# Kernel optimization log

Hardware: AMD Instinct MI355X
Metric: run time of the kernel (lower is better)

Reference implementation:

```python
import jax, jax.numpy as jnp
import numpy as np

N_SPLIT = 4096   # split tokens (coarse octree levels)
N_VQ    = 12288  # VQ tokens (finest level)
N       = N_SPLIT + N_VQ
C       = 256    # num_embed
H       = 8      # num_heads
L       = 4      # num_blocks
P       = 256    # patch_size (attention window)
DIL     = 2      # dilation for odd (swin) blocks
DVQ     = 32     # vqvae embedding_channels
VQ_SIZE = 256    # vqvae embedding_sizes
VQ_G    = 4      # vqvae quantizer_group
HID     = 4 * C


def _layernorm(x, s, b):
    m = x.mean(-1, keepdims=True)
    v = jnp.var(x, axis=-1, keepdims=True)
    return (x - m) * jax.lax.rsqrt(v + 1e-5) * s + b


def _sin_pos_emb(n, c):
    pos = jnp.arange(n, dtype=jnp.float32)[:, None]
    half = c // 2
    freqs = jnp.exp(-jnp.log(10000.0) * jnp.arange(half, dtype=jnp.float32) / half)
    ang = pos * freqs
    return jnp.concatenate([jnp.sin(ang), jnp.cos(ang)], axis=-1)


def _forward(split, zq, targets_vq, category, batch_id, mask, d2b,
             split_emb, class_emb, vq_proj_w, vq_proj_b,
             ln1_s, ln1_b, qkv_w, qkv_b, attn_w, attn_b,
             ln2_s, ln2_b, fc1_w, fc1_b, fc2_w, fc2_b,
             lnx_s, lnx_b, split_w, split_b, vq_w, vq_b):
    # token embeddings: [split tokens ; projected VQ codes]
    x = jnp.concatenate([split_emb[split], zq @ vq_proj_w + vq_proj_b], axis=0)  # [N,C]
    cond = class_emb[category]                      # [B,C]
    x = jnp.where(mask[:, None], cond[batch_id], x)  # masked tokens -> class cond

    # depth2batch gather, then OctFormer blocks
    xb = x[d2b] + _sin_pos_emb(N, C).astype(x.dtype)
    dh = C // H
    scale = dh ** -0.5
    for l in range(L):
        d = DIL if (l % 2 == 1) else 1  # swin-style alternating dilation
        h = _layernorm(xb, ln1_s[l], ln1_b[l])
        # dilated window partition: window j in a super-window holds tokens base+p*d+j
        hw = h.reshape(-1, P, d, C).transpose(0, 2, 1, 3).reshape(-1, P, C)
        qkv = hw @ qkv_w[l] + qkv_b[l]              # [nw,P,3C]
        q, k, v = [t.reshape(-1, P, H, dh) for t in jnp.split(qkv, 3, axis=-1)]
        att = jax.nn.softmax(jnp.einsum('wphd,wqhd->whpq', q, k) * scale, axis=-1)
        o = jnp.einsum('whpq,wqhd->wphd', att, v).reshape(-1, P, C) @ attn_w[l] + attn_b[l]
        o = o.reshape(-1, d, P, C).transpose(0, 2, 1, 3).reshape(-1, C)  # undo partition
        xb = xb + o
        h = _layernorm(xb, ln2_s[l], ln2_b[l])
        xb = xb + (jax.nn.gelu(h @ fc1_w[l] + fc1_b[l]) @ fc2_w[l] + fc2_b[l])
    # batch2depth scatter (inverse permutation)
    x = jnp.zeros_like(xb).at[d2b].set(xb)
    x = _layernorm(x, lnx_s, lnx_b)

    # split head + masked cross-entropy
    sl = x[:N_SPLIT] @ split_w + split_b            # [Ns,2]
    ms = mask[:N_SPLIT].astype(jnp.float32)
    ce_s = -jnp.take_along_axis(jax.nn.log_softmax(sl, axis=-1), split[:, None], axis=-1)[:, 0]
    split_loss = jnp.sum(ce_s * ms) / jnp.maximum(jnp.sum(ms), 1.0)

    # vq head + masked grouped cross-entropy
    vl = (x[N_SPLIT:] @ vq_w + vq_b).reshape(N_VQ, VQ_G, VQ_SIZE)
    mv = mask[N_SPLIT:].astype(jnp.float32)
    ce_v = -jnp.take_along_axis(jax.nn.log_softmax(vl, axis=-1), targets_vq[..., None], axis=-1)[..., 0]
    vq_loss = jnp.sum(ce_v.mean(-1) * mv) / jnp.maximum(jnp.sum(mv), 1.0)
    return jnp.stack([split_loss, vq_loss])


def setup_inputs() -> dict:
    key = jax.random.key(0)
    ks = jax.random.split(key, 16)
    s = 0.02
    inp = {
        'split': jax.random.randint(ks[0], (N_SPLIT,), 0, 2),
        'zq': jax.random.normal(ks[1], (N_VQ, DVQ), jnp.float32),
        'targets_vq': jax.random.randint(ks[2], (N_VQ, VQ_G), 0, VQ_SIZE),
        'category': jnp.zeros((1,), jnp.int32),
        'batch_id': jnp.zeros((N,), jnp.int32),
        'mask': jax.random.randint(ks[3], (N,), 0, 2).astype(bool),
        'd2b': jax.random.permutation(ks[4], N),
        'split_emb': s * jax.random.normal(ks[5], (2, C), jnp.float32),
        'class_emb': s * jax.random.normal(ks[6], (1, C), jnp.float32),
        'vq_proj_w': s * jax.random.normal(ks[7], (DVQ, C), jnp.float32),
        'vq_proj_b': jnp.zeros((C,), jnp.float32),
        'ln1_s': jnp.ones((L, C), jnp.float32),
        'ln1_b': jnp.zeros((L, C), jnp.float32),
        'qkv_w': s * jax.random.normal(ks[8], (L, C, 3 * C), jnp.float32),
        'qkv_b': jnp.zeros((L, 3 * C), jnp.float32),
        'attn_w': s * jax.random.normal(ks[9], (L, C, C), jnp.float32),
        'attn_b': jnp.zeros((L, C), jnp.float32),
        'ln2_s': jnp.ones((L, C), jnp.float32),
        'ln2_b': jnp.zeros((L, C), jnp.float32),
        'fc1_w': s * jax.random.normal(ks[10], (L, C, HID), jnp.float32),
        'fc1_b': jnp.zeros((L, HID), jnp.float32),
        'fc2_w': s * jax.random.normal(ks[11], (L, HID, C), jnp.float32),
        'fc2_b': jnp.zeros((L, C), jnp.float32),
        'lnx_s': jnp.ones((C,), jnp.float32),
        'lnx_b': jnp.zeros((C,), jnp.float32),
        'split_w': s * jax.random.normal(ks[12], (C, 2), jnp.float32),
        'split_b': jnp.zeros((2,), jnp.float32),
        'vq_w': s * jax.random.normal(ks[13], (C, VQ_G * VQ_SIZE), jnp.float32),
        'vq_b': jnp.zeros((VQ_G * VQ_SIZE,), jnp.float32),
    }
    return inp


def reference(split, zq, targets_vq, category, batch_id, mask, d2b,
              split_emb, class_emb, vq_proj_w, vq_proj_b,
              ln1_s, ln1_b, qkv_w, qkv_b, attn_w, attn_b,
              ln2_s, ln2_b, fc1_w, fc1_b, fc2_w, fc2_b,
              lnx_s, lnx_b, split_w, split_b, vq_w, vq_b):
    return _forward(split, zq, targets_vq, category, batch_id, mask, d2b,
                    split_emb, class_emb, vq_proj_w, vq_proj_b,
                    ln1_s, ln1_b, qkv_w, qkv_b, attn_w, attn_b,
                    ln2_s, ln2_b, fc1_w, fc1_b, fc2_w, fc2_b,
                    lnx_s, lnx_b, split_w, split_b, vq_w, vq_b)
```

## Files before the change

### kernel.cpp

```cpp
#include <hip/hip_runtime.h>
#include <hip/hip_bf16.h>
#include <math.h>

#define NSPLIT 4096
#define NVQ    12288
#define NTOK   16384
#define CH     256
#define NH     8
#define DHD    32
#define NL     4
#define PW     256
#define HIDN   1024
#define DVQ    32
#define VQG    4
#define VQS    256

typedef __attribute__((ext_vector_type(8))) short bf16x8;
typedef __attribute__((ext_vector_type(4))) float f32x4;

typedef const __attribute__((address_space(1))) void* gas_ptr;
typedef __attribute__((address_space(3))) void* las_ptr;
#define GLD16(g, s) __builtin_amdgcn_global_load_lds((gas_ptr)(g), (las_ptr)(s), 16, 0, 0)

static __device__ __forceinline__ unsigned pack2bf(float a, float b) {
    __hip_bfloat16 ha = __float2bfloat16(a), hb = __float2bfloat16(b);
    return ((unsigned)*(unsigned short*)&hb << 16) | *(unsigned short*)&ha;
}
static __device__ __forceinline__ float bf2f(unsigned short s) {
    unsigned u = (unsigned)s << 16;
    return *(float*)&u;
}
static __device__ __forceinline__ unsigned short f2bfu(float f) {
    __hip_bfloat16 h = __float2bfloat16(f);
    return *(unsigned short*)&h;
}

__global__ void k_mask(const void* __restrict__ raw, int* __restrict__ mi) {
    __shared__ int c_even, c_odd, c_0100, sh_mode;
    const unsigned short* u16 = (const unsigned short*)raw;
    if (threadIdx.x == 0) { c_even = 0; c_odd = 0; c_0100 = 0; }
    __syncthreads();
    int le = 0, lo = 0, l01 = 0;
    for (int i = threadIdx.x; i < 8192; i += 256) {
        unsigned short v = u16[i];
        if (v == 0x3F80u) { if (i & 1) lo++; else le++; }
        if (v == 0x0100u) l01++;
    }
    atomicAdd(&c_even, le); atomicAdd(&c_odd, lo); atomicAdd(&c_0100, l01);
    __syncthreads();
    if (threadIdx.x == 0) {
        int m;
        if      (c_even > 500) m = 2;
        else if (c_odd  > 500) m = 3;
        else if (c_0100 > 500) m = 1;
        else                   m = 0;
        sh_mode = m;
    }
    __syncthreads();
    int m = sh_mode;
    for (int i = threadIdx.x; i < NTOK; i += 256) {
        int v;
        if      (m == 0) v = ((const int*)raw)[i] != 0;
        else if (m == 1) v = ((const unsigned char*)raw)[i] != 0;
        else if (m == 2) v = ((const unsigned short*)raw)[i] != 0;
        else             v = ((const unsigned int*)raw)[i] != 0;
        mi[i] = v;
    }
}

__global__ void k_wt_all(const float* __restrict__ qkv_w, const float* __restrict__ attn_w,
                         const float* __restrict__ fc1_w, const float* __restrict__ fc2_w,
                         const float* __restrict__ vq_w,
                         short* __restrict__ qkvT, short* __restrict__ attnT,
                         short* __restrict__ fc1T, short* __restrict__ fc2T,
                         short* __restrict__ vqT) {
    int b = blockIdx.x;
    const float* W; short* Wt; int K, N, tn, tk;
    if (b < 192)      { int r = b;       int z = r / 48; r %= 48; K = 256;  N = 768;
                        tk = r / 12; tn = r % 12;
                        W = qkv_w + (size_t)z * K * N; Wt = qkvT + (size_t)z * K * N; }
    else if (b < 256) { int r = b - 192; int z = r / 16; r %= 16; K = 256;  N = 256;
                        tk = r / 4;  tn = r % 4;
                        W = attn_w + (size_t)z * K * N; Wt = attnT + (size_t)z * K * N; }
    else if (b < 512) { int r = b - 256; int z = r / 64; r %= 64; K = 256;  N = 1024;
                        tk = r / 16; tn = r % 16;
                        W = fc1_w + (size_t)z * K * N; Wt = fc1T + (size_t)z * K * N; }
    else if (b < 768) { int r = b - 512; int z = r / 64; r %= 64; K = 1024; N = 256;
                        tk = r / 4;  tn = r % 4;
                        W = fc2_w + (size_t)z * K * N; Wt = fc2T + (size_t)z * K * N; }
    else              { int r = b - 768; K = 256; N = 1024;
                        tk = r / 16; tn = r % 16; W = vq_w; Wt = vqT; }
    __shared__ float t[64][65];
    int bn = tn * 64, bk = tk * 64, tid = threadIdx.x;
#pragma unroll
    for (int it = 0; it < 16; ++it) {
        int idx = it * 256 + tid; int r = idx >> 6, c = idx & 63;
        t[r][c] = W[(size_t)(bk + r) * N + bn + c];
    }
    __syncthreads();
#pragma unroll
    for (int it = 0; it < 16; ++it) {
        int idx = it * 256 + tid; int r = idx >> 6, c = idx & 63;
        __hip_bfloat16 h = __float2bfloat16(t[c][r]);
        Wt[(size_t)(bn + r) * K + bk + c] = *(short*)&h;
    }
}

__global__ void k_embed_gather(const int* __restrict__ split, const float* __restrict__ zq,
                               const int* __restrict__ category, const int* __restrict__ batch_id,
                               const int* __restrict__ mask_i, const int* __restrict__ d2b,
                               const float* __restrict__ split_emb, const float* __restrict__ class_emb,
                               const float* __restrict__ vq_proj_w, const float* __restrict__ vq_proj_b,
                               const float* __restrict__ ln1s, const float* __restrict__ ln1b,
                               unsigned short* __restrict__ xbv, unsigned short* __restrict__ hb) {
    int j = blockIdx.x, c = threadIdx.x;
    int i = d2b[j];
    float v;
    if (mask_i[i]) {
        v = class_emb[category[batch_id[i]] * CH + c];
    } else if (i < NSPLIT) {
        v = split_emb[split[i] * CH + c];
    } else {
        const float* z = zq + (size_t)(i - NSPLIT) * DVQ;
        float acc = vq_proj_b[c];
#pragma unroll
        for (int k = 0; k < DVQ; k++) acc += z[k] * vq_proj_w[k * CH + c];
        v = acc;
    }
    const float kneg = -0.07195578415606394f;
    float jf = (float)j, pe;
    if (c < 128) { float f = expf(c * kneg);         pe = sinf(jf * f); }
    else         { float f = expf((c - 128) * kneg); pe = cosf(jf * f); }
    v += pe;
    float s = v, sq = v * v;
#pragma unroll
    for (int o = 32; o; o >>= 1) { s += __shfl_xor(s, o); sq += __shfl_xor(sq, o); }
    __shared__ float ps[4], pq[4];
    if ((c & 63) == 0) { ps[c >> 6] = s; pq[c >> 6] = sq; }
    __syncthreads();
    float S = ps[0] + ps[1] + ps[2] + ps[3];
    float Q = pq[0] + pq[1] + pq[2] + pq[3];
    float mean = S * (1.0f / CH);
    float var  = Q * (1.0f / CH) - mean * mean;
    float rsf = rsqrtf(var + 1e-5f);
    xbv[(size_t)j * CH + c] = f2bfu(v);
    hb[(size_t)j * CH + c]  = f2bfu((v - mean) * rsf * ln1s[c] + ln1b[c]);
}

template <int GELU>
__global__ __launch_bounds__(256, 4) void k_mm(
    const short* __restrict__ A, const short* __restrict__ Bt,
    const float* __restrict__ bias, __hip_bfloat16* __restrict__ outB,
    int N, int K) {
    __shared__ short As[2][128 * 32];
    __shared__ short Bs[2][128 * 32];
    const int tid = threadIdx.x;
    const int w = tid >> 6, l = tid & 63;
    const int bm = blockIdx.y * 128, bn = blockIdx.x * 128;
    const int wr = w >> 1, wc = w & 1;
    const int q = l >> 4, rA = l & 15;
    const int srow = w * 16 + (l >> 2);
    const int sx = ((l & 3) ^ ((l >> 2) & 3)) * 8;
    const int fx = (q ^ (rA & 3)) * 8;

    const short* gA0 = A + (size_t)(bm + srow) * K + sx;
    const short* gA1 = A + (size_t)(bm + srow + 64) * K + sx;
    const short* gB0 = Bt + (size_t)(bn + srow) * K + sx;
    const short* gB1 = Bt + (size_t)(bn + srow + 64) * K + sx;
    short* lA0 = &As[0][w * 16 * 32];
    short* lA1 = &As[0][(64 + w * 16) * 32];
    short* lA0h = &As[1][w * 16 * 32];
    short* lA1h = &As[1][(64 + w * 16) * 32];
    short* lB0 = &Bs[0][w * 16 * 32];
    short* lB1 = &Bs[0][(64 + w * 16) * 32];
    short* lB0h = &Bs[1][w * 16 * 32];
    short* lB1h = &Bs[1][(64 + w * 16) * 32];

    f32x4 acc[4][4] = {};

    for (int k0 = 0; k0 < K; k0 += 64) {
        GLD16(gA0 + k0, lA0);       GLD16(gA1 + k0, lA1);
        GLD16(gA0 + k0 + 32, lA0h); GLD16(gA1 + k0 + 32, lA1h);
        GLD16(gB0 + k0, lB0);       GLD16(gB1 + k0, lB1);
        GLD16(gB0 + k0 + 32, lB0h); GLD16(gB1 + k0 + 32, lB1h);
        __syncthreads();
#pragma unroll
        for (int s = 0; s < 2; s++) {
            bf16x8 a[4], b[4];
#pragma unroll
            for (int m = 0; m < 4; m++)
                a[m] = *(const bf16x8*)(&As[s][(wr * 64 + m * 16 + rA) * 32 + fx]);
#pragma unroll
            for (int n = 0; n < 4; n++)
                b[n] = *(const bf16x8*)(&Bs[s][(wc * 64 + n * 16 + rA) * 32 + fx]);
#pragma unroll
            for (int m = 0; m < 4; m++)
#pragma unroll
                for (int n = 0; n < 4; n++)
                    acc[m][n] = __builtin_amdgcn_mfma_f32_16x16x32_bf16(a[m], b[n], acc[m][n], 0, 0, 0);
        }
        __syncthreads();
    }

#pragma unroll
    for (int m = 0; m < 4; m++) {
        int row0 = bm + wr * 64 + m * 16 + q * 4;
#pragma unroll
        for (int n = 0; n < 4; n++) {
            int col = bn + wc * 64 + n * 16 + rA;
            float bv = bias[col];
#pragma unroll
            for (int r2 = 0; r2 < 4; r2++) {
                float v = acc[m][n][r2] + bv;
                if (GELU) {
                    float t = tanhf(0.7978845608028654f * (v + 0.044715f * v * v * v));
                    v = 0.5f * v * (1.0f + t);
                }
                outB[(size_t)(row0 + r2) * N + col] = __float2bfloat16(v);
            }
        }
    }
}

template <int LNOUT>
__global__ __launch_bounds__(256, 3) void k_mm_row(
    const short* __restrict__ A, const short* __restrict__ Bt,
    const float* __restrict__ bias, unsigned short* __restrict__ xbv,
    const float* __restrict__ lns, const float* __restrict__ lnb,
    unsigned short* __restrict__ h_out, int K) {
    __shared__ short As[2][64 * 32];
    __shared__ short Bs[2][256 * 32];
    __shared__ float part[2][4][64];
    const int tid = threadIdx.x;
    const int w = tid >> 6, l = tid & 63;
    const int bm = blockIdx.x * 64;
    const int q = l >> 4, rA = l & 15;
    const int sx = ((l & 3) ^ ((l >> 2) & 3)) * 8;
    const int fx = (q ^ (rA & 3)) * 8;

    const short* gA = A + (size_t)(bm + w * 16 + (l >> 2)) * K + sx;
    const short* gB = Bt + (size_t)(w * 64 + (l >> 2)) * K + sx;
    short* lA0 = &As[0][(w * 16) * 32];
    short* lA1 = &As[1][(w * 16) * 32];

    f32x4 acc[4][4] = {};

    for (int k0 = 0; k0 < K; k0 += 64) {
        GLD16(gA + k0, lA0);
        GLD16(gA + k0 + 32, lA1);
#pragma unroll
        for (int i = 0; i < 4; i++) {
            GLD16(gB + (size_t)(i * 16) * K + k0,      &Bs[0][(w * 64 + i * 16) * 32]);
            GLD16(gB + (size_t)(i * 16) * K + k0 + 32, &Bs[1][(w * 64 + i * 16) * 32]);
        }
        __syncthreads();
#pragma unroll
        for (int s = 0; s < 2; s++) {
            bf16x8 a[4], b[4];
#pragma unroll
            for (int m = 0; m < 4; m++)
                a[m] = *(const bf16x8*)(&As[s][(m * 16 + rA) * 32 + fx]);
#pragma unroll
            for (int n = 0; n < 4; n++)
                b[n] = *(const bf16x8*)(&Bs[s][(w * 64 + n * 16 + rA) * 32 + fx]);
#pragma unroll
            for (int m = 0; m < 4; m++)
#pragma unroll
                for (int n = 0; n < 4; n++)
                    acc[m][n] = __builtin_amdgcn_mfma_f32_16x16x32_bf16(a[m], b[n], acc[m][n], 0, 0, 0);
        }
        __syncthreads();
    }

    float rsum[4][4] = {}, rsq[4][4] = {};
#pragma unroll
    for (int m = 0; m < 4; m++) {
#pragma unroll
        for (int n = 0; n < 4; n++) {
            int col = w * 64 + n * 16 + rA;
            float bv = bias[col];
#pragma unroll
            for (int r2 = 0; r2 < 4; r2++) {
                int row = bm + m * 16 + q * 4 + r2;
                size_t oi = (size_t)row * CH + col;
                float v = acc[m][n][r2] + bv + bf2f(xbv[oi]);
                acc[m][n][r2] = v;
                xbv[oi] = f2bfu(v);
                rsum[m][r2] += v;
                rsq[m][r2] += v * v;
            }
        }
    }
    if (LNOUT) {
#pragma unroll
        for (int m = 0; m < 4; m++)
#pragma unroll
            for (int r2 = 0; r2 < 4; r2++) {
#pragma unroll
                for (int o = 8; o; o >>= 1) {
                    rsum[m][r2] += __shfl_xor(rsum[m][r2], o);
                    rsq[m][r2]  += __shfl_xor(rsq[m][r2], o);
                }
            }
        if (rA == 0) {
#pragma unroll
            for (int m = 0; m < 4; m++)
#pragma unroll
                for (int r2 = 0; r2 < 4; r2++) {
                    int row = m * 16 + q * 4 + r2;
                    part[0][w][row] = rsum[m][r2];
                    part[1][w][row] = rsq[m][r2];
                }
        }
        __syncthreads();
#pragma unroll
        for (int m = 0; m < 4; m++) {
#pragma unroll
            for (int r2 = 0; r2 < 4; r2++) {
                int row = m * 16 + q * 4 + r2;
                float S = part[0][0][row] + part[0][1][row] + part[0][2][row] + part[0][3][row];
                float Q = part[1][0][row] + part[1][1][row] + part[1][2][row] + part[1][3][row];
                float mean = S * (1.0f / CH);
                float var  = Q * (1.0f / CH) - mean * mean;
                float rsf = rsqrtf(var + 1e-5f);
#pragma unroll
                for (int n = 0; n < 4; n++) {
                    int col = w * 64 + n * 16 + rA;
                    float h = (acc[m][n][r2] - mean) * rsf * lns[col] + lnb[col];
                    h_out[(size_t)(bm + row) * CH + col] = f2bfu(h);
                }
            }
        }
    }
}

__global__ __launch_bounds__(256) void k_attn_mfma(const short* __restrict__ qkv,
                                                   short* __restrict__ o, int dil) {
    __shared__ short Vt[DHD * PW];
    __shared__ short Pl[4][64 * 64];
    const int wid = blockIdx.x, h = blockIdx.y;
    const int tid = threadIdx.x;
    const int w = tid >> 6, l = tid & 63;
    const int g = l >> 4, c = l & 15;
    const int tbase = (wid / dil) * (PW * dil) + (wid % dil);

    {
        const int p = tid;
        const short* src = qkv + (size_t)(tbase + p * dil) * 768 + 2 * CH + h * DHD;
        bf16x8 v0 = *(const bf16x8*)(src);
        bf16x8 v1 = *(const bf16x8*)(src + 8);
        bf16x8 v2 = *(const bf16x8*)(src + 16);
        bf16x8 v3 = *(const bf16x8*)(src + 24);
        const int pc = p >> 3, po = p & 7;
#pragma unroll
        for (int d = 0; d < 8; d++)  Vt[(d)      * PW + ((pc ^ d) << 3) + po] = v0[d];
#pragma unroll
        for (int d = 0; d < 8; d++)  Vt[(d + 8)  * PW + ((pc ^ d) << 3) + po] = v1[d];
#pragma unroll
        for (int d = 0; d < 8; d++)  Vt[(d + 16) * PW + ((pc ^ d) << 3) + po] = v2[d];
#pragma unroll
        for (int d = 0; d < 8; d++)  Vt[(d + 24) * PW + ((pc ^ d) << 3) + po] = v3[d];
    }

    bf16x8 qf[4];
#pragma unroll
    for (int qt = 0; qt < 4; qt++) {
        int qrow = w * 64 + qt * 16 + c;
        qf[qt] = *(const bf16x8*)(qkv + (size_t)(tbase + qrow * dil) * 768 + h * DHD + g * 8);
    }

    f32x4 acco[4][2] = {};
    float m_s[4] = {-1e30f, -1e30f, -1e30f, -1e30f};
    float l_s[4] = {0.f, 0.f, 0.f, 0.f};
    const float scale = 0.17677669529663687f;

    __syncthreads();

#pragma unroll
    for (int ch = 0; ch < 4; ch++) {
        bf16x8 kf[4];
#pragma unroll
        for (int kvt = 0; kvt < 4; kvt++) {
            int kv = ch * 64 + kvt * 16 + c;
            kf[kvt] = *(const bf16x8*)(qkv + (size_t)(tbase + kv * dil) * 768 + CH + h * DHD + g * 8);
        }
        f32x4 accs[4][4] = {};
#pragma unroll
        for (int kvt = 0; kvt < 4; kvt++)
#pragma unroll
            for (int qt = 0; qt < 4; qt++)
                accs[kvt][qt] = __builtin_amdgcn_mfma_f32_16x16x32_bf16(kf[kvt], qf[qt], accs[kvt][qt], 0, 0, 0);

        float fb[4];
#pragma unroll
        for (int qt = 0; qt < 4; qt++) {
            float mx = -1e30f;
#pragma unroll
            for (int kvt = 0; kvt < 4; kvt++) {
                mx = fmaxf(mx, fmaxf(fmaxf(accs[kvt][qt][0], accs[kvt][qt][1]),
                                     fmaxf(accs[kvt][qt][2], accs[kvt][qt][3])));
            }
            mx = fmaxf(mx, __shfl_xor(mx, 16));
            mx = fmaxf(mx, __shfl_xor(mx, 32));
            float mnew = fmaxf(m_s[qt], mx * scale);
            fb[qt] = __expf(m_s[qt] - mnew);
            m_s[qt] = mnew;
        }
#pragma unroll
        for (int mt = 0; mt < 4; mt++)
#pragma unroll
            for (int r = 0; r < 4; r++) {
                float fo = __shfl(fb[mt], g * 4 + r);
                acco[mt][0][r] *= fo;
                acco[mt][1][r] *= fo;
            }
        float rsum[4] = {0.f, 0.f, 0.f, 0.f};
#pragma unroll
        for (int kvt = 0; kvt < 4; kvt++) {
            const int cchunk = kvt * 2 + (g >> 1);
            const int koff = (g & 1) << 2;
#pragma unroll
            for (int qt = 0; qt < 4; qt++) {
                float p0 = __expf(accs[kvt][qt][0] * scale - m_s[qt]);
                float p1 = __expf(accs[kvt][qt][1] * scale - m_s[qt]);
                float p2 = __expf(accs[kvt][qt][2] * scale - m_s[qt]);
                float p3 = __expf(accs[kvt][qt][3] * scale - m_s[qt]);
                rsum[qt] += (p0 + p1) + (p2 + p3);
                int qq = qt * 16 + c;
                int phys = cchunk ^ (qq & 7);
                uint2 pk; pk.x = pack2bf(p0, p1); pk.y = pack2bf(p2, p3);
                *(uint2*)(&Pl[w][qq * 64 + phys * 8 + koff]) = pk;
            }
        }
#pragma unroll
        for (int qt = 0; qt < 4; qt++) {
            float s = rsum[qt];
            s += __shfl_xor(s, 16);
            s += __shfl_xor(s, 32);
            l_s[qt] = l_s[qt] * fb[qt] + s;
        }
#pragma unroll
        for (int ks = 0; ks < 2; ks++) {
            bf16x8 pa[4];
#pragma unroll
            for (int mt = 0; mt < 4; mt++) {
                int qq = mt * 16 + c;
                int phys = (ks * 4 + g) ^ (qq & 7);
                pa[mt] = *(const bf16x8*)(&Pl[w][qq * 64 + phys * 8]);
            }
#pragma unroll
            for (int nt = 0; nt < 2; nt++) {
                int d = nt * 16 + c;
                int kvabs = ch * 64 + ks * 32 + g * 8;
                int phys = (kvabs >> 3) ^ (d & 7);
                bf16x8 vb = *(const bf16x8*)(&Vt[d * PW + phys * 8]);
#pragma unroll
                for (int mt = 0; mt < 4; mt++)
                    acco[mt][nt] = __builtin_amdgcn_mfma_f32_16x16x32_bf16(pa[mt], vb, acco[mt][nt], 0, 0, 0);
            }
        }
    }

#pragma unroll
    for (int mt = 0; mt < 4; mt++) {
        float linv_own = 1.0f / l_s[mt];
#pragma unroll
        for (int r = 0; r < 4; r++) {
            float linv = __shfl(linv_own, g * 4 + r);
            int qrow = w * 64 + mt * 16 + g * 4 + r;
            size_t trow = (size_t)(tbase + qrow * dil) * CH + h * DHD;
#pragma unroll
            for (int nt = 0; nt < 2; nt++) {
                __hip_bfloat16 hv = __float2bfloat16(acco[mt][nt][r] * linv);
                o[trow + nt * 16 + c] = *(short*)&hv;
            }
        }
    }
}

__global__ void k_lnx_scatter_split(const unsigned short* __restrict__ xbv, const int* __restrict__ d2b,
                                    const float* __restrict__ s, const float* __restrict__ b,
                                    const int* __restrict__ split, const int* __restrict__ mask_i,
                                    const float* __restrict__ sw, const float* __restrict__ sb,
                                    __hip_bfloat16* __restrict__ out,
                                    float* __restrict__ sce, float* __restrict__ smv) {
    int j = blockIdx.x * 4 + (threadIdx.x >> 6);
    int l = threadIdx.x & 63;
    ushort4 uv = *(const ushort4*)(xbv + (size_t)j * CH + l * 4);
    float vx = bf2f(uv.x), vy = bf2f(uv.y), vz = bf2f(uv.z), vw = bf2f(uv.w);
    float sum = vx + vy + vz + vw;
    float sq  = vx * vx + vy * vy + vz * vz + vw * vw;
#pragma unroll
    for (int o = 32; o; o >>= 1) { sum += __shfl_xor(sum, o); sq += __shfl_xor(sq, o); }
    float mean = sum * (1.0f / CH);
    float var  = sq * (1.0f / CH) - mean * mean;
    float rs = rsqrtf(var + 1e-5f);
    float4 sv = *(const float4*)(s + l * 4);
    float4 bv = *(const float4*)(b + l * 4);
    float n0 = (vx - mean) * rs * sv.x + bv.x;
    float n1 = (vy - mean) * rs * sv.y + bv.y;
    float n2 = (vz - mean) * rs * sv.z + bv.z;
    float n3 = (vw - mean) * rs * sv.w + bv.w;
    int i = d2b[j];
    uint2 pk; pk.x = pack2bf(n0, n1); pk.y = pack2bf(n2, n3);
    *(uint2*)((unsigned short*)out + (size_t)i * CH + l * 4) = pk;
    if (i < NSPLIT) {
        int c0 = l * 4;
        float a0 = n0 * sw[2 * c0] + n1 * sw[2 * (c0 + 1)] + n2 * sw[2 * (c0 + 2)] + n3 * sw[2 * (c0 + 3)];
        float a1 = n0 * sw[2 * c0 + 1] + n1 * sw[2 * (c0 + 1) + 1] + n2 * sw[2 * (c0 + 2) + 1] + n3 * sw[2 * (c0 + 3) + 1];
#pragma unroll
        for (int o = 32; o; o >>= 1) { a0 += __shfl_xor(a0, o); a1 += __shfl_xor(a1, o); }
        if (l == 0) {
            float l0 = a0 + sb[0], l1 = a1 + sb[1];
            float mx = fmaxf(l0, l1);
            float lse = mx + logf(__expf(l0 - mx) + __expf(l1 - mx));
            float ce = lse - (split[i] ? l1 : l0);
            float ms = (float)mask_i[i];
            sce[i] = ce * ms;
            smv[i] = ms;
        }
    }
}

__global__ void k_vq_loss(const unsigned short* __restrict__ vl, const int* __restrict__ targets,
                          const int* __restrict__ mask_i, float* __restrict__ vce,
                          float* __restrict__ vmv) {
    int i = blockIdx.x;
    int wv = threadIdx.x >> 6;
    int l = threadIdx.x & 63;
    const unsigned short* row = vl + (size_t)i * (VQG * VQS) + wv * VQS;
    ushort4 v4 = *(const ushort4*)(row + l * 4);
    float e0 = bf2f(v4.x), e1 = bf2f(v4.y), e2 = bf2f(v4.z), e3 = bf2f(v4.w);
    float mx = fmaxf(fmaxf(e0, e1), fmaxf(e2, e3));
#pragma unroll
    for (int o = 32; o; o >>= 1) mx = fmaxf(mx, __shfl_xor(mx, o));
    float s = __expf(e0 - mx) + __expf(e1 - mx) + __expf(e2 - mx) + __expf(e3 - mx);
#pragma unroll
    for (int o = 32; o; o >>= 1) s += __shfl_xor(s, o);
    __shared__ float ce[VQG];
    if (l == 0) ce[wv] = (mx + logf(s)) - bf2f(row[targets[i * VQG + wv]]);
    __syncthreads();
    if (threadIdx.x == 0) {
        float mv = (float)mask_i[NSPLIT + i];
        vce[i] = (ce[0] + ce[1] + ce[2] + ce[3]) * 0.25f * mv;
        vmv[i] = mv;
    }
}

__global__ void k_reduce(const float* __restrict__ sce, const float* __restrict__ smv,
                         const float* __restrict__ vce, const float* __restrict__ vmv,
                         float* __restrict__ out) {
    int tid = threadIdx.x;
    float s1 = 0, s2 = 0, s3 = 0, s4 = 0;
    for (int i = tid; i < NSPLIT; i += 256) { s1 += sce[i]; s2 += smv[i]; }
    for (int i = tid; i < NVQ; i += 256)    { s3 += vce[i]; s4 += vmv[i]; }
    __shared__ float r1[256], r2[256], r3[256], r4[256];
    r1[tid] = s1; r2[tid] = s2; r3[tid] = s3; r4[tid] = s4;
    __syncthreads();
    for (int o = 128; o; o >>= 1) {
        if (tid < o) { r1[tid] += r1[tid + o]; r2[tid] += r2[tid + o];
                       r3[tid] += r3[tid + o]; r4[tid] += r4[tid + o]; }
        __syncthreads();
    }
    if (tid == 0) {
        out[0] = r1[0] / fmaxf(r2[0], 1.0f);
        out[1] = r3[0] / fmaxf(r4[0], 1.0f);
    }
}

extern "C" void kernel_launch(void* const* d_in, const int* in_sizes, int n_in,
                              void* d_out, int out_size, void* d_ws, size_t ws_size,
                              hipStream_t stream) {
    const int*   split      = (const int*)d_in[0];
    const float* zq         = (const float*)d_in[1];
    const int*   targets_vq = (const int*)d_in[2];
    const int*   category   = (const int*)d_in[3];
    const int*   batch_id   = (const int*)d_in[4];
    const void*  mask_raw   = d_in[5];
    const int*   d2b        = (const int*)d_in[6];
    const float* split_emb  = (const float*)d_in[7];
    const float* class_emb  = (const float*)d_in[8];
    const float* vq_proj_w  = (const float*)d_in[9];
    const float* vq_proj_b  = (const float*)d_in[10];
    const float* ln1_s      = (const float*)d_in[11];
    const float* ln1_b      = (const float*)d_in[12];
    const float* qkv_w      = (const float*)d_in[13];
    const float* qkv_b      = (const float*)d_in[14];
    const float* attn_w     = (const float*)d_in[15];
    const float* attn_b     = (const float*)d_in[16];
    const float* ln2_s      = (const float*)d_in[17];
    const float* ln2_b      = (const float*)d_in[18];
    const float* fc1_w      = (const float*)d_in[19];
    const float* fc1_b      = (const float*)d_in[20];
    const float* fc2_w      = (const float*)d_in[21];
    const float* fc2_b      = (const float*)d_in[22];
    const float* lnx_s      = (const float*)d_in[23];
    const float* lnx_b      = (const float*)d_in[24];
    const float* sw         = (const float*)d_in[25];
    const float* sb         = (const float*)d_in[26];
    const float* vq_w       = (const float*)d_in[27];
    const float* vq_b       = (const float*)d_in[28];

    char* ws = (char*)d_ws;
    int* mask_i = (int*)(ws + 256);
    float* sce = (float*)(ws + 256 + 4 * NTOK);
    float* smv = sce + NSPLIT;
    float* vce = smv + NSPLIT;
    float* vmv = vce + NVQ;
    char* p = ws + (1 << 20);
    short* qkvT = (short*)p;  p += (size_t)NL * 768 * CH * 2;
    short* attnT = (short*)p; p += (size_t)NL * CH * CH * 2;
    short* fc1T = (short*)p;  p += (size_t)NL * HIDN * CH * 2;
    short* fc2T = (short*)p;  p += (size_t)NL * CH * HIDN * 2;
    short* vqT = (short*)p;   p += (size_t)HIDN * CH * 2;
    unsigned short* xbv = (unsigned short*)p; p += (size_t)NTOK * CH * 2;
    unsigned short* h_bf = (unsigned short*)p; p += (size_t)NTOK * CH * 2;
    unsigned short* o_bf = (unsigned short*)p; p += (size_t)NTOK * CH * 2;
    short* big = (short*)p;

    k_mask<<<1, 256, 0, stream>>>(mask_raw, mask_i);
    k_wt_all<<<832, 256, 0, stream>>>(qkv_w, attn_w, fc1_w, fc2_w, vq_w,
                                      qkvT, attnT, fc1T, fc2T, vqT);
    k_embed_gather<<<NTOK, 256, 0, stream>>>(split, zq, category, batch_id, mask_i, d2b,
                                             split_emb, class_emb, vq_proj_w, vq_proj_b,
                                             ln1_s, ln1_b, xbv, h_bf);

    for (int l = 0; l < NL; l++) {
        int d = (l & 1) ? 2 : 1;
        k_mm<0><<<dim3(768 / 128, NTOK / 128), 256, 0, stream>>>(
            (const short*)h_bf, qkvT + (size_t)l * 768 * CH, qkv_b + l * 768,
            (__hip_bfloat16*)big, 768, CH);
        k_attn_mfma<<<dim3(NTOK / PW, NH), 256, 0, stream>>>(big, (short*)o_bf, d);
        k_mm_row<1><<<NTOK / 64, 256, 0, stream>>>(
            (const short*)o_bf, attnT + (size_t)l * CH * CH, attn_b + l * CH,
            xbv, ln2_s + l * CH, ln2_b + l * CH, h_bf, CH);
        k_mm<1><<<dim3(HIDN / 128, NTOK / 128), 256, 0, stream>>>(
            (const short*)h_bf, fc1T + (size_t)l * HIDN * CH, fc1_b + l * HIDN,
            (__hip_bfloat16*)big, HIDN, CH);
        if (l < NL - 1) {
            k_mm_row<1><<<NTOK / 64, 256, 0, stream>>>(
                big, fc2T + (size_t)l * CH * HIDN, fc2_b + l * CH,
                xbv, ln1_s + (l + 1) * CH, ln1_b + (l + 1) * CH, h_bf, HIDN);
        } else {
            k_mm_row<0><<<NTOK / 64, 256, 0, stream>>>(
                big, fc2T + (size_t)l * CH * HIDN, fc2_b + l * CH,
                xbv, nullptr, nullptr, nullptr, HIDN);
        }
    }

    k_lnx_scatter_split<<<NTOK / 4, 256, 0, stream>>>(xbv, d2b, lnx_s, lnx_b, split, mask_i,
                                                      sw, sb, (__hip_bfloat16*)h_bf, sce, smv);
    k_mm<0><<<dim3(HIDN / 128, NVQ / 128), 256, 0, stream>>>(
        (const short*)(h_bf + (size_t)NSPLIT * CH), vqT, vq_b,
        (__hip_bfloat16*)big, HIDN, CH);
    k_vq_loss<<<NVQ, 256, 0, stream>>>((const unsigned short*)big, targets_vq, mask_i, vce, vmv);
    k_reduce<<<1, 256, 0, stream>>>(sce, smv, vce, vmv, (float*)d_out);
}
```

Baseline: 521.9 us.

## Fold mask decoding into existing kernels and stage K tiles in LDS for attention

Removes the standalone single-block mask kernel. Its mode detection now runs in an extra block of the weight-transpose kernel, and the per-token mask decode runs inside the embed-gather kernel, which saves a serial launch. The attention kernel also loads its K head slice into LDS through an XOR swizzle with async global-to-LDS loads instead of reading K from global memory on every kv chunk. This adds 16KB of LDS per block, which may reduce occupancy.

```diff
diff --git a/kernel.cpp b/kernel.cpp
--- a/kernel.cpp
+++ b/kernel.cpp
@@ -35,46 +35,37 @@
     return *(unsigned short*)&h;
 }
 
-__global__ void k_mask(const void* __restrict__ raw, int* __restrict__ mi) {
-    __shared__ int c_even, c_odd, c_0100, sh_mode;
-    const unsigned short* u16 = (const unsigned short*)raw;
-    if (threadIdx.x == 0) { c_even = 0; c_odd = 0; c_0100 = 0; }
-    __syncthreads();
-    int le = 0, lo = 0, l01 = 0;
-    for (int i = threadIdx.x; i < 8192; i += 256) {
-        unsigned short v = u16[i];
-        if (v == 0x3F80u) { if (i & 1) lo++; else le++; }
-        if (v == 0x0100u) l01++;
-    }
-    atomicAdd(&c_even, le); atomicAdd(&c_odd, lo); atomicAdd(&c_0100, l01);
-    __syncthreads();
-    if (threadIdx.x == 0) {
-        int m;
-        if      (c_even > 500) m = 2;
-        else if (c_odd  > 500) m = 3;
-        else if (c_0100 > 500) m = 1;
-        else                   m = 0;
-        sh_mode = m;
-    }
-    __syncthreads();
-    int m = sh_mode;
-    for (int i = threadIdx.x; i < NTOK; i += 256) {
-        int v;
-        if      (m == 0) v = ((const int*)raw)[i] != 0;
-        else if (m == 1) v = ((const unsigned char*)raw)[i] != 0;
-        else if (m == 2) v = ((const unsigned short*)raw)[i] != 0;
-        else             v = ((const unsigned int*)raw)[i] != 0;
-        mi[i] = v;
-    }
-}
-
 __global__ void k_wt_all(const float* __restrict__ qkv_w, const float* __restrict__ attn_w,
                          const float* __restrict__ fc1_w, const float* __restrict__ fc2_w,
                          const float* __restrict__ vq_w,
                          short* __restrict__ qkvT, short* __restrict__ attnT,
                          short* __restrict__ fc1T, short* __restrict__ fc2T,
-                         short* __restrict__ vqT) {
+                         short* __restrict__ vqT,
+                         const void* __restrict__ mask_raw, int* __restrict__ mode) {
     int b = blockIdx.x;
+    if (b == 832) {
+        __shared__ int c_even, c_odd, c_0100;
+        const unsigned short* u16 = (const unsigned short*)mask_raw;
+        if (threadIdx.x == 0) { c_even = 0; c_odd = 0; c_0100 = 0; }
+        __syncthreads();
+        int le = 0, lo = 0, l01 = 0;
+        for (int i = threadIdx.x; i < 8192; i += 256) {
+            unsigned short v = u16[i];
+            if (v == 0x3F80u) { if (i & 1) lo++; else le++; }
+            if (v == 0x0100u) l01++;
+        }
+        atomicAdd(&c_even, le); atomicAdd(&c_odd, lo); atomicAdd(&c_0100, l01);
+        __syncthreads();
+        if (threadIdx.x == 0) {
+            int m;
+            if      (c_even > 500) m = 2;
+            else if (c_odd  > 500) m = 3;
+            else if (c_0100 > 500) m = 1;
+            else                   m = 0;
+            *mode = m;
+        }
+        return;
+    }
     const float* W; short* Wt; int K, N, tn, tk;
     if (b < 192)      { int r = b;       int z = r / 48; r %= 48; K = 256;  N = 768;
                         tk = r / 12; tn = r % 12;
@@ -108,15 +99,22 @@
 
 __global__ void k_embed_gather(const int* __restrict__ split, const float* __restrict__ zq,
                                const int* __restrict__ category, const int* __restrict__ batch_id,
-                               const int* __restrict__ mask_i, const int* __restrict__ d2b,
+                               const void* __restrict__ mask_raw, const int* __restrict__ mode,
+                               int* __restrict__ mask_i, const int* __restrict__ d2b,
                                const float* __restrict__ split_emb, const float* __restrict__ class_emb,
                                const float* __restrict__ vq_proj_w, const float* __restrict__ vq_proj_b,
                                const float* __restrict__ ln1s, const float* __restrict__ ln1b,
                                unsigned short* __restrict__ xbv, unsigned short* __restrict__ hb) {
     int j = blockIdx.x, c = threadIdx.x;
     int i = d2b[j];
+    int m = *mode, mv;
+    if      (m == 0) mv = ((const int*)mask_raw)[i] != 0;
+    else if (m == 1) mv = ((const unsigned char*)mask_raw)[i] != 0;
+    else if (m == 2) mv = ((const unsigned short*)mask_raw)[i] != 0;
+    else             mv = ((const unsigned int*)mask_raw)[i] != 0;
+    if (c == 0) mask_i[i] = mv;
     float v;
-    if (mask_i[i]) {
+    if (mv) {
         v = class_emb[category[batch_id[i]] * CH + c];
     } else if (i < NSPLIT) {
         v = split_emb[split[i] * CH + c];
@@ -337,12 +335,21 @@
 __global__ __launch_bounds__(256) void k_attn_mfma(const short* __restrict__ qkv,
                                                    short* __restrict__ o, int dil) {
     __shared__ short Vt[DHD * PW];
+    __shared__ short Kl[PW * DHD];
     __shared__ short Pl[4][64 * 64];
     const int wid = blockIdx.x, h = blockIdx.y;
     const int tid = threadIdx.x;
     const int w = tid >> 6, l = tid & 63;
     const int g = l >> 4, c = l & 15;
     const int tbase = (wid / dil) * (PW * dil) + (wid % dil);
+
+#pragma unroll
+    for (int j2 = 0; j2 < 4; j2++) {
+        int row = j2 * 64 + w * 16 + (l >> 2);
+        int sc = (l & 3) ^ (row & 3);
+        GLD16(qkv + (size_t)(tbase + row * dil) * 768 + CH + h * DHD + sc * 8,
+              Kl + (j2 * 64 + w * 16) * DHD);
+    }
 
     {
         const int p = tid;
@@ -382,7 +389,7 @@
 #pragma unroll
         for (int kvt = 0; kvt < 4; kvt++) {
             int kv = ch * 64 + kvt * 16 + c;
-            kf[kvt] = *(const bf16x8*)(qkv + (size_t)(tbase + kv * dil) * 768 + CH + h * DHD + g * 8);
+            kf[kvt] = *(const bf16x8*)(Kl + kv * DHD + ((g ^ (c & 3)) * 8));
         }
         f32x4 accs[4][4] = {};
 #pragma unroll
@@ -602,6 +609,7 @@
     const float* vq_b       = (const float*)d_in[28];
 
     char* ws = (char*)d_ws;
+    int* mode   = (int*)ws;
     int* mask_i = (int*)(ws + 256);
     float* sce = (float*)(ws + 256 + 4 * NTOK);
     float* smv = sce + NSPLIT;
@@ -618,12 +626,11 @@
     unsigned short* o_bf = (unsigned short*)p; p += (size_t)NTOK * CH * 2;
     short* big = (short*)p;
 
-    k_mask<<<1, 256, 0, stream>>>(mask_raw, mask_i);
-    k_wt_all<<<832, 256, 0, stream>>>(qkv_w, attn_w, fc1_w, fc2_w, vq_w,
-                                      qkvT, attnT, fc1T, fc2T, vqT);
-    k_embed_gather<<<NTOK, 256, 0, stream>>>(split, zq, category, batch_id, mask_i, d2b,
-                                             split_emb, class_emb, vq_proj_w, vq_proj_b,
-                                             ln1_s, ln1_b, xbv, h_bf);
+    k_wt_all<<<833, 256, 0, stream>>>(qkv_w, attn_w, fc1_w, fc2_w, vq_w,
+                                      qkvT, attnT, fc1T, fc2T, vqT, mask_raw, mode);
+    k_embed_gather<<<NTOK, 256, 0, stream>>>(split, zq, category, batch_id, mask_raw, mode,
+                                             mask_i, d2b, split_emb, class_emb,
+                                             vq_proj_w, vq_proj_b, ln1_s, ln1_b, xbv, h_bf);
 
     for (int l = 0; l < NL; l++) {
         int d = (l & 1) ? 2 : 1;
```

New measurement: 501.7 us. 1.04x faster.
